# Kernel optimization log

Measured on AMD Instinct MI355X. Metric: run time of the kernel, lower is better.

## Reference

```python
import jax, jax.numpy as jnp
import numpy as np

N_FFT = 1024
HOP = 256
F_BINS = N_FFT // 2 + 1  # 513


def _make_dft_kernel():
    # torch.hann_window(N) is periodic: 0.5*(1 - cos(2*pi*k/N))
    window = 0.5 * (1.0 - np.cos(2.0 * np.pi * np.arange(N_FFT) / N_FFT))
    # rfft of identity, transposed -> (F, n_fft), then apply window along time axis
    dftm = np.fft.rfft(np.eye(N_FFT)).T * window[None, :]  # complex (F, n_fft)
    # view_as_real + rearrange 'f n ri -> (ri f) n': real block first, imag block second
    kernel = np.concatenate([dftm.real, dftm.imag], axis=0)  # (2F, n_fft)
    return jnp.asarray(kernel, dtype=jnp.float32)


def setup_inputs() -> dict:
    key = jax.random.key(0)
    signal = jax.random.normal(key, (16, 262144), dtype=jnp.float32)
    kernel = _make_dft_kernel()  # (1026, 1024) fixed windowed-DFT matrix (buffer)
    return {"signal": signal, "kernel": kernel}


def reference(signal, kernel):
    # center=True: reflect-pad by n_fft//2 on both sides
    pad = N_FFT // 2
    x = jnp.pad(signal, ((0, 0), (pad, pad)), mode="reflect")  # (B, L)
    B, L = x.shape
    n_frames = (L - N_FFT) // HOP + 1
    # im2col framing: (n_frames, n_fft) gather indices
    idx = jnp.arange(n_frames)[:, None] * HOP + jnp.arange(N_FFT)[None, :]
    frames = x[:, idx]  # (B, n_frames, n_fft)
    # conv1d as GEMM: (B, 2F, n_frames)
    out = jnp.einsum("btn,cn->bct", frames, kernel)
    # rearrange '(ri f) n -> f n ri' with ri outer
    out = out.reshape(B, 2, F_BINS, n_frames)
    return jnp.transpose(out, (0, 2, 3, 1))  # (B, F, n_frames, 2)
```

## Files before the change

kernel.cpp:

```cpp
#include <hip/hip_runtime.h>
#include <hip/hip_bf16.h>
#include <cstdint>


#define HOP 256
#define NFFT 1024
#define FB 513
#define NT 1025
#define NBATCH 16
#define MCH 1026
#define MP2 1280
#define SIGLEN 262144
#define SIGP 263168
#define BM 256
#define BN 128
#define BK 32
#define NKT 32
#define A_BYTES 16384
#define B_BYTES 8192
#define SLOT_BYTES (A_BYTES + B_BYTES)

typedef __attribute__((ext_vector_type(8))) short short8;
typedef __attribute__((ext_vector_type(4))) float f32x4;
typedef unsigned int u32;

__device__ __forceinline__ unsigned short f2bf(float f) {
  u32 u = __float_as_uint(f);
  u = (u + 0x7FFFu + ((u >> 16) & 1u)) >> 16;
  return (unsigned short)u;
}
__device__ __forceinline__ float bf2f(unsigned short s) {
  return __uint_as_float(((u32)s) << 16);
}

__global__ __launch_bounds__(256) void prep_A(const float* __restrict__ kern,
                                              unsigned short* __restrict__ A) {
  size_t i8 = ((size_t)blockIdx.x * 256 + threadIdx.x) * 8;
  int row = (int)(i8 >> 10);
  int col = (int)(i8 & 1023);
  short8 v = {0, 0, 0, 0, 0, 0, 0, 0};
  if (row < MCH) {
    int f = row >> 1, ri = row & 1;
    int src_row = ri * FB + f;
    const float* s = kern + ((size_t)src_row << 10) + col;
#pragma unroll
    for (int e = 0; e < 8; ++e) v[e] = (short)f2bf(s[e]);
  }
  *(short8*)(A + i8) = v;
}

__global__ __launch_bounds__(256) void prep_S(const float* __restrict__ sig,
                                              unsigned short* __restrict__ S) {
  size_t i8 = ((size_t)blockIdx.x * 256 + threadIdx.x) * 8;
  int b = (int)(i8 / SIGP);
  int i = (int)(i8 - (size_t)b * SIGP);
  const float* sb = sig + (size_t)b * SIGLEN;
  short8 v;
#pragma unroll
  for (int e = 0; e < 8; ++e) {
    int j = i + e - 512;
    j = (j < 0) ? -j : j;
    j = (j >= SIGLEN) ? (2 * SIGLEN - 2 - j) : j;
    v[e] = (short)f2bf(sb[j]);
  }
  *(short8*)(S + i8) = v;
}

__device__ __forceinline__ void async16(void* lds, const void* g) {
  __builtin_amdgcn_global_load_lds(
      (const __attribute__((address_space(1))) u32*)g,
      (__attribute__((address_space(3))) u32*)lds, 16, 0, 0);
}

__global__ __launch_bounds__(512, 4) void stft_mm(const unsigned short* __restrict__ A,
                                                  const unsigned short* __restrict__ S,
                                                  float* __restrict__ out) {
  __shared__ __align__(16) char smem[2][SLOT_BYTES];

  const int tid = threadIdx.x;
  const int lane = tid & 63;
  const int wid = tid >> 6;
  const int wr = wid >> 1;
  const int wc = wid & 1;
  const int lr = lane & 15;
  const int g16 = lane >> 4;

  const int bid = blockIdx.x;
  const int wg = (bid & 7) * 64 + (bid >> 3);
  const int mt = wg & 3;
  const int r2 = wg >> 2;
  const int nt = r2 & 7;
  const int b  = r2 >> 3;

  const int c0 = mt * BM;
  const int t0 = nt * BN;

  const char* Ab = (const char*)A;
  const char* Sb = (const char*)(S + (size_t)b * SIGP);

#define STAGE_TILE(kt, s)                                                      \
  {                                                                            \
    char* As_ = &smem[s][0];                                                   \
    char* Bs_ = &smem[s][A_BYTES];                                             \
    _Pragma("unroll") for (int j = 0; j < 2; ++j) {                            \
      const int G0 = j * 512 + wid * 64;                                       \
      u32 p = (u32)(G0 + lane) * 16u;                                          \
      u32 q = p ^ (((p >> 7) & 3u) << 4);                                      \
      const char* src = Ab + ((size_t)(c0 + (int)(q >> 6)) << 11)              \
                           + (kt) * 64 + (int)(q & 63u);                       \
      async16(As_ + (size_t)G0 * 16u, src);                                    \
    }                                                                          \
    {                                                                          \
      const int G0 = wid * 64;                                                 \
      u32 p = (u32)(G0 + lane) * 16u;                                          \
      u32 q = p ^ (((p >> 7) & 3u) << 4);                                      \
      const char* src = Sb + ((size_t)(t0 + (int)(q >> 6)) << 9)               \
                           + (kt) * 64 + (int)(q & 63u);                       \
      async16(Bs_ + (size_t)G0 * 16u, src);                                    \
    }                                                                          \
  }

  STAGE_TILE(0, 0)
  __syncthreads();

  u32 pa[4], pb[4];
#pragma unroll
  for (int mi = 0; mi < 4; ++mi) {
    u32 q = (u32)((wr * 64 + mi * 16 + lr) * 64 + g16 * 16);
    pa[mi] = q ^ (((q >> 7) & 3u) << 4);
  }
#pragma unroll
  for (int ni = 0; ni < 4; ++ni) {
    u32 q = (u32)((wc * 64 + ni * 16 + lr) * 64 + g16 * 16);
    pb[ni] = q ^ (((q >> 7) & 3u) << 4);
  }

  f32x4 acc[4][4] = {};

#pragma unroll
  for (int k = 0; k < NKT; ++k) {
    const char* As = &smem[k & 1][0];
    const char* Bs = As + A_BYTES;

    if (k + 1 < NKT) STAGE_TILE(k + 1, (k + 1) & 1)

    short8 af[4], bfv[4];
#pragma unroll
    for (int mi = 0; mi < 4; ++mi) af[mi] = *(const short8*)(As + pa[mi]);
#pragma unroll
    for (int ni = 0; ni < 4; ++ni) bfv[ni] = *(const short8*)(Bs + pb[ni]);

#pragma unroll
    for (int mi = 0; mi < 4; ++mi)
#pragma unroll
      for (int ni = 0; ni < 4; ++ni)
        acc[mi][ni] = __builtin_amdgcn_mfma_f32_16x16x32_bf16(
            af[mi], bfv[ni], acc[mi][ni], 0, 0, 0);

    if (k + 1 < NKT) __syncthreads();
  }
#undef STAGE_TILE

#pragma unroll
  for (int mi = 0; mi < 4; ++mi) {
    const int cb = c0 + wr * 64 + mi * 16 + g16 * 4;
    const int f0 = cb >> 1;
#pragma unroll
    for (int ni = 0; ni < 4; ++ni) {
      const int t = t0 + wc * 64 + ni * 16 + lr;
      *(float2*)(out + ((((size_t)b * FB + f0) * NT + t) << 1)) =
          make_float2(acc[mi][ni][0], acc[mi][ni][1]);
      *(float2*)(out + ((((size_t)b * FB + f0 + 1) * NT + t) << 1)) =
          make_float2(acc[mi][ni][2], acc[mi][ni][3]);
    }
  }
}

__global__ __launch_bounds__(256) void stft_edge(const unsigned short* __restrict__ A,
                                                 const unsigned short* __restrict__ S,
                                                 float* __restrict__ out) {
  const int wv = blockIdx.x * 4 + (threadIdx.x >> 6);
  const int lane = threadIdx.x & 63;
  int b, f, t;
  if (wv < NBATCH * NT) {
    b = wv / NT; t = wv - b * NT; f = FB - 1;
  } else {
    int u = wv - NBATCH * NT;
    b = u / FB; f = u - b * FB; t = NT - 1;
  }
  const unsigned short* w  = S + (size_t)b * SIGP + (size_t)t * HOP + lane * 16;
  const unsigned short* r0 = A + ((size_t)(2 * f) << 10) + lane * 16;
  const unsigned short* r1 = r0 + 1024;
  short8 wv0 = *(const short8*)w,  wv1 = *(const short8*)(w + 8);
  short8 a0  = *(const short8*)r0, a1  = *(const short8*)(r0 + 8);
  short8 b0  = *(const short8*)r1, b1  = *(const short8*)(r1 + 8);
  float d0 = 0.f, d1 = 0.f;
#pragma unroll
  for (int e = 0; e < 8; ++e) {
    float x0 = bf2f((unsigned short)wv0[e]), x1 = bf2f((unsigned short)wv1[e]);
    d0 += bf2f((unsigned short)a0[e]) * x0 + bf2f((unsigned short)a1[e]) * x1;
    d1 += bf2f((unsigned short)b0[e]) * x0 + bf2f((unsigned short)b1[e]) * x1;
  }
#pragma unroll
  for (int m = 32; m; m >>= 1) {
    d0 += __shfl_xor(d0, m);
    d1 += __shfl_xor(d1, m);
  }
  if (lane == 0)
    *(float2*)(out + ((((size_t)b * FB + f) * NT + t) << 1)) = make_float2(d0, d1);
}

extern "C" void kernel_launch(void* const* d_in, const int* in_sizes, int n_in,
                              void* d_out, int out_size, void* d_ws, size_t ws_size,
                              hipStream_t stream) {
  const float* sig = (const float*)d_in[0];
  const float* kern = (const float*)d_in[1];
  float* out = (float*)d_out;

  unsigned short* wsA = (unsigned short*)d_ws;
  unsigned short* wsS = wsA + (size_t)MP2 * NFFT;

  prep_A<<<dim3(MP2 * NFFT / 8 / 256), 256, 0, stream>>>(kern, wsA);
  prep_S<<<dim3(NBATCH * SIGP / 8 / 256), 256, 0, stream>>>(sig, wsS);
  stft_mm<<<dim3(4 * 8 * NBATCH), 512, 0, stream>>>(wsA, wsS, out);
  stft_edge<<<dim3((NBATCH * NT + NBATCH * FB) / 4), 256, 0, stream>>>(wsA, wsS, out);
}
```

Measured before the change: 69.71 us.

## Triple-buffer GEMM pipeline and fuse prep and edge kernels into fewer launches

Merges the two preprocessing kernels into one launch and folds the edge-row/column dot-product work into the main GEMM launch as extra blocks. The GEMM's LDS pipeline goes from two to three stages, prefetching two tiles ahead with explicit vmcnt waits and raw barriers instead of __syncthreads. This aims to cut launch overhead and hide global-load latency. In exchange, LDS use per block rises to 72KB, which limits occupancy, and edge blocks also reserve that dynamic LDS.

```diff
diff --git a/kernel.cpp b/kernel.cpp
--- a/kernel.cpp
+++ b/kernel.cpp
@@ -16,9 +16,12 @@
 #define BN 128
 #define BK 32
 #define NKT 32
-#define A_BYTES 16384
-#define B_BYTES 8192
-#define SLOT_BYTES (A_BYTES + B_BYTES)
+#define A_T 16384
+#define B_T 8192
+#define SLOT_BYTES (A_T + B_T)
+#define LDS_BYTES (3 * SLOT_BYTES)
+#define NMAIN 512
+#define NEDGE 3076
 
 typedef __attribute__((ext_vector_type(8))) short short8;
 typedef __attribute__((ext_vector_type(4))) float f32x4;
@@ -33,37 +36,39 @@
   return __uint_as_float(((u32)s) << 16);
 }
 
-__global__ __launch_bounds__(256) void prep_A(const float* __restrict__ kern,
-                                              unsigned short* __restrict__ A) {
-  size_t i8 = ((size_t)blockIdx.x * 256 + threadIdx.x) * 8;
-  int row = (int)(i8 >> 10);
-  int col = (int)(i8 & 1023);
-  short8 v = {0, 0, 0, 0, 0, 0, 0, 0};
-  if (row < MCH) {
-    int f = row >> 1, ri = row & 1;
-    int src_row = ri * FB + f;
-    const float* s = kern + ((size_t)src_row << 10) + col;
-#pragma unroll
-    for (int e = 0; e < 8; ++e) v[e] = (short)f2bf(s[e]);
-  }
-  *(short8*)(A + i8) = v;
-}
-
-__global__ __launch_bounds__(256) void prep_S(const float* __restrict__ sig,
-                                              unsigned short* __restrict__ S) {
-  size_t i8 = ((size_t)blockIdx.x * 256 + threadIdx.x) * 8;
-  int b = (int)(i8 / SIGP);
-  int i = (int)(i8 - (size_t)b * SIGP);
-  const float* sb = sig + (size_t)b * SIGLEN;
-  short8 v;
-#pragma unroll
-  for (int e = 0; e < 8; ++e) {
-    int j = i + e - 512;
-    j = (j < 0) ? -j : j;
-    j = (j >= SIGLEN) ? (2 * SIGLEN - 2 - j) : j;
-    v[e] = (short)f2bf(sb[j]);
-  }
-  *(short8*)(S + i8) = v;
+#define NA_BLK 640
+#define NS_BLK 2056
+__global__ __launch_bounds__(256) void prep_all(const float* __restrict__ kern,
+                                                const float* __restrict__ sig,
+                                                unsigned short* __restrict__ A,
+                                                unsigned short* __restrict__ S) {
+  if (blockIdx.x < NA_BLK) {
+    size_t i8 = ((size_t)blockIdx.x * 256 + threadIdx.x) * 8;
+    int row = (int)(i8 >> 10);
+    int col = (int)(i8 & 1023);
+    short8 v = {0, 0, 0, 0, 0, 0, 0, 0};
+    if (row < MCH) {
+      int f = row >> 1, ri = row & 1;
+      const float* s = kern + ((size_t)(ri * FB + f) << 10) + col;
+#pragma unroll
+      for (int e = 0; e < 8; ++e) v[e] = (short)f2bf(s[e]);
+    }
+    *(short8*)(A + i8) = v;
+  } else {
+    size_t i8 = ((size_t)(blockIdx.x - NA_BLK) * 256 + threadIdx.x) * 8;
+    int b = (int)(i8 / SIGP);
+    int i = (int)(i8 - (size_t)b * SIGP);
+    const float* sb = sig + (size_t)b * SIGLEN;
+    short8 v;
+#pragma unroll
+    for (int e = 0; e < 8; ++e) {
+      int j = i + e - 512;
+      j = (j < 0) ? -j : j;
+      j = (j >= SIGLEN) ? (2 * SIGLEN - 2 - j) : j;
+      v[e] = (short)f2bf(sb[j]);
+    }
+    *(short8*)(S + i8) = v;
+  }
 }
 
 __device__ __forceinline__ void async16(void* lds, const void* g) {
@@ -75,17 +80,50 @@
 __global__ __launch_bounds__(512, 4) void stft_mm(const unsigned short* __restrict__ A,
                                                   const unsigned short* __restrict__ S,
                                                   float* __restrict__ out) {
-  __shared__ __align__(16) char smem[2][SLOT_BYTES];
+  extern __shared__ char smem[];
 
   const int tid = threadIdx.x;
   const int lane = tid & 63;
   const int wid = tid >> 6;
+  const int bid = blockIdx.x;
+
+  if (bid >= NMAIN) {
+    const int wv = (bid - NMAIN) * 8 + wid;
+    int b, f, t;
+    if (wv < NBATCH * NT) {
+      b = wv / NT; t = wv - b * NT; f = FB - 1;
+    } else {
+      int u = wv - NBATCH * NT;
+      b = u / FB; f = u - b * FB; t = NT - 1;
+    }
+    const unsigned short* w  = S + (size_t)b * SIGP + (size_t)t * HOP + lane * 16;
+    const unsigned short* r0 = A + ((size_t)(2 * f) << 10) + lane * 16;
+    const unsigned short* r1 = r0 + 1024;
+    short8 wv0 = *(const short8*)w,  wv1 = *(const short8*)(w + 8);
+    short8 a0  = *(const short8*)r0, a1  = *(const short8*)(r0 + 8);
+    short8 b0  = *(const short8*)r1, b1  = *(const short8*)(r1 + 8);
+    float d0 = 0.f, d1 = 0.f;
+#pragma unroll
+    for (int e = 0; e < 8; ++e) {
+      float x0 = bf2f((unsigned short)wv0[e]), x1 = bf2f((unsigned short)wv1[e]);
+      d0 += bf2f((unsigned short)a0[e]) * x0 + bf2f((unsigned short)a1[e]) * x1;
+      d1 += bf2f((unsigned short)b0[e]) * x0 + bf2f((unsigned short)b1[e]) * x1;
+    }
+#pragma unroll
+    for (int m = 32; m; m >>= 1) {
+      d0 += __shfl_xor(d0, m);
+      d1 += __shfl_xor(d1, m);
+    }
+    if (lane == 0)
+      *(float2*)(out + ((((size_t)b * FB + f) * NT + t) << 1)) = make_float2(d0, d1);
+    return;
+  }
+
   const int wr = wid >> 1;
   const int wc = wid & 1;
   const int lr = lane & 15;
   const int g16 = lane >> 4;
 
-  const int bid = blockIdx.x;
   const int wg = (bid & 7) * 64 + (bid >> 3);
   const int mt = wg & 3;
   const int r2 = wg >> 2;
@@ -100,8 +138,8 @@
 
 #define STAGE_TILE(kt, s)                                                      \
   {                                                                            \
-    char* As_ = &smem[s][0];                                                   \
-    char* Bs_ = &smem[s][A_BYTES];                                             \
+    char* As_ = smem + (s) * SLOT_BYTES;                                       \
+    char* Bs_ = As_ + A_T;                                                     \
     _Pragma("unroll") for (int j = 0; j < 2; ++j) {                            \
       const int G0 = j * 512 + wid * 64;                                       \
       u32 p = (u32)(G0 + lane) * 16u;                                          \
@@ -121,7 +159,10 @@
   }
 
   STAGE_TILE(0, 0)
-  __syncthreads();
+  STAGE_TILE(1, 1)
+  asm volatile("s_waitcnt vmcnt(3)" ::: "memory");
+  __builtin_amdgcn_s_barrier();
+  asm volatile("" ::: "memory");
 
   u32 pa[4], pb[4];
 #pragma unroll
@@ -139,16 +180,16 @@
 
 #pragma unroll
   for (int k = 0; k < NKT; ++k) {
-    const char* As = &smem[k & 1][0];
-    const char* Bs = As + A_BYTES;
-
-    if (k + 1 < NKT) STAGE_TILE(k + 1, (k + 1) & 1)
+    const char* As = smem + (k % 3) * SLOT_BYTES;
+    const char* Bs = As + A_T;
 
     short8 af[4], bfv[4];
 #pragma unroll
     for (int mi = 0; mi < 4; ++mi) af[mi] = *(const short8*)(As + pa[mi]);
 #pragma unroll
     for (int ni = 0; ni < 4; ++ni) bfv[ni] = *(const short8*)(Bs + pb[ni]);
+
+    if (k + 2 < NKT) STAGE_TILE(k + 2, (k + 2) % 3)
 
 #pragma unroll
     for (int mi = 0; mi < 4; ++mi)
@@ -157,7 +198,12 @@
         acc[mi][ni] = __builtin_amdgcn_mfma_f32_16x16x32_bf16(
             af[mi], bfv[ni], acc[mi][ni], 0, 0, 0);
 
-    if (k + 1 < NKT) __syncthreads();
+    if (k + 1 < NKT) {
+      if (k <= NKT - 3) asm volatile("s_waitcnt vmcnt(3)" ::: "memory");
+      else              asm volatile("s_waitcnt vmcnt(0)" ::: "memory");
+      __builtin_amdgcn_s_barrier();
+      asm volatile("" ::: "memory");
+    }
   }
 #undef STAGE_TILE
 
@@ -176,40 +222,6 @@
   }
 }
 
-__global__ __launch_bounds__(256) void stft_edge(const unsigned short* __restrict__ A,
-                                                 const unsigned short* __restrict__ S,
-                                                 float* __restrict__ out) {
-  const int wv = blockIdx.x * 4 + (threadIdx.x >> 6);
-  const int lane = threadIdx.x & 63;
-  int b, f, t;
-  if (wv < NBATCH * NT) {
-    b = wv / NT; t = wv - b * NT; f = FB - 1;
-  } else {
-    int u = wv - NBATCH * NT;
-    b = u / FB; f = u - b * FB; t = NT - 1;
-  }
-  const unsigned short* w  = S + (size_t)b * SIGP + (size_t)t * HOP + lane * 16;
-  const unsigned short* r0 = A + ((size_t)(2 * f) << 10) + lane * 16;
-  const unsigned short* r1 = r0 + 1024;
-  short8 wv0 = *(const short8*)w,  wv1 = *(const short8*)(w + 8);
-  short8 a0  = *(const short8*)r0, a1  = *(const short8*)(r0 + 8);
-  short8 b0  = *(const short8*)r1, b1  = *(const short8*)(r1 + 8);
-  float d0 = 0.f, d1 = 0.f;
-#pragma unroll
-  for (int e = 0; e < 8; ++e) {
-    float x0 = bf2f((unsigned short)wv0[e]), x1 = bf2f((unsigned short)wv1[e]);
-    d0 += bf2f((unsigned short)a0[e]) * x0 + bf2f((unsigned short)a1[e]) * x1;
-    d1 += bf2f((unsigned short)b0[e]) * x0 + bf2f((unsigned short)b1[e]) * x1;
-  }
-#pragma unroll
-  for (int m = 32; m; m >>= 1) {
-    d0 += __shfl_xor(d0, m);
-    d1 += __shfl_xor(d1, m);
-  }
-  if (lane == 0)
-    *(float2*)(out + ((((size_t)b * FB + f) * NT + t) << 1)) = make_float2(d0, d1);
-}
-
 extern "C" void kernel_launch(void* const* d_in, const int* in_sizes, int n_in,
                               void* d_out, int out_size, void* d_ws, size_t ws_size,
                               hipStream_t stream) {
@@ -220,8 +232,9 @@
   unsigned short* wsA = (unsigned short*)d_ws;
   unsigned short* wsS = wsA + (size_t)MP2 * NFFT;
 
-  prep_A<<<dim3(MP2 * NFFT / 8 / 256), 256, 0, stream>>>(kern, wsA);
-  prep_S<<<dim3(NBATCH * SIGP / 8 / 256), 256, 0, stream>>>(sig, wsS);
-  stft_mm<<<dim3(4 * 8 * NBATCH), 512, 0, stream>>>(wsA, wsS, out);
-  stft_edge<<<dim3((NBATCH * NT + NBATCH * FB) / 4), 256, 0, stream>>>(wsA, wsS, out);
-}
+  (void)hipFuncSetAttribute((const void*)stft_mm,
+                            hipFuncAttributeMaxDynamicSharedMemorySize, LDS_BYTES);
+
+  prep_all<<<dim3(NA_BLK + NS_BLK), 256, 0, stream>>>(kern, sig, wsA, wsS);
+  stft_mm<<<dim3(NMAIN + NEDGE), 512, LDS_BYTES, stream>>>(wsA, wsS, out);
+}
```

Result: slower. 82.27 us (+18.0%).
